# Performance work log

Hardware: AMD Instinct MI355X
Metric: run time of the kernel (lower is better)

## Reference

```python
import jax, jax.numpy as jnp
import numpy as np

B, S, E, H = 8, 1024, 1024, 16
D = E // H  # head_dim = hidden_size // num_heads


def setup_inputs() -> dict:
    key = jax.random.key(0)
    ks = jax.random.split(key, 9)
    s = 0.02
    return {
        "h":  jax.random.normal(ks[0], (B, S, E), jnp.float32),
        # per-head projection weights stacked over heads; torch Linear(E, D) -> stored [E, D] (x @ W)
        "Wq": jax.random.normal(ks[1], (H, E, D), jnp.float32) * s,
        "bq": jax.random.normal(ks[2], (H, D), jnp.float32) * s,
        "Wk": jax.random.normal(ks[3], (H, E, D), jnp.float32) * s,
        "bk": jax.random.normal(ks[4], (H, D), jnp.float32) * s,
        "Wv": jax.random.normal(ks[5], (H, E, D), jnp.float32) * s,  # dead weight: original passes h as value
        "bv": jax.random.normal(ks[6], (H, D), jnp.float32) * s,
        "Wo": jax.random.normal(ks[7], (E, E), jnp.float32) * s,
        "bo": jax.random.normal(ks[8], (E,), jnp.float32) * s,
    }


def reference(h, Wq, bq, Wk, bk, Wv, bv, Wo, bo):
    # Batched over all heads at once instead of the original Python loop.
    q = jnp.einsum('bse,hed->bhsd', h, Wq) + bq[None, :, None, :]   # [B,H,S,D]
    k = jnp.einsum('bse,hed->bhsd', h, Wk) + bk[None, :, None, :]   # [B,H,S,D]
    # v is computed in the original module but NOT used (do_attention gets h as value)
    _v = jnp.einsum('bse,hed->bhsd', h, Wv) + bv[None, :, None, :]
    scale = 1.0 / jnp.sqrt(jnp.asarray(D, h.dtype))
    scores = jnp.einsum('bhsd,bhtd->bhst', q, k) * scale            # [B,H,S,T]
    # original: F.softmax(scores, dim=1) on per-head [B,S,T] -> query axis = axis 2 here
    weights = jax.nn.softmax(scores, axis=2)
    ctx = jnp.einsum('bhst,bte->bhse', weights, h)                  # value = h (embed_dim), per original
    # torch.cat over dim=1 of per-head [B,S,E] outputs -> [B, H*S, E]
    x = ctx.reshape(B, H * S, E)
    return x @ Wo + bo
```

## Files before the change

kernel.cpp:

```cpp
#include <hip/hip_runtime.h>

#define B_ 8
#define S_ 1024
#define E_ 1024
#define H_ 16
#define D_ 64

typedef __attribute__((ext_vector_type(8))) __bf16 bf16x8;
typedef __attribute__((ext_vector_type(4))) float f32x4;
typedef __attribute__((ext_vector_type(4))) unsigned short u16x4;
typedef __attribute__((ext_vector_type(8))) unsigned short u16x8;

static __device__ __forceinline__ unsigned short f2bf_hw(float f) {
  union { __bf16 b; unsigned short u; } v;
  v.b = (__bf16)f;
  return v.u;
}

#if __has_builtin(__builtin_amdgcn_exp2f)
#define EXP2(x) __builtin_amdgcn_exp2f(x)
#else
#define EXP2(x) exp2f(x)
#endif
#define SCALE2 0.18033688f

#define MFMA16(a, b, c) __builtin_amdgcn_mfma_f32_16x16x32_bf16((a), (b), (c), 0, 0, 0)

__global__ void cast_f32_bf16_kernel(const float* __restrict__ src,
                                     unsigned short* __restrict__ dst, int n4) {
  int i = blockIdx.x * 256 + threadIdx.x;
  if (i >= n4) return;
  float4 v = reinterpret_cast<const float4*>(src)[i];
  u16x4 o;
  o[0] = f2bf_hw(v.x); o[1] = f2bf_hw(v.y); o[2] = f2bf_hw(v.z); o[3] = f2bf_hw(v.w);
  reinterpret_cast<u16x4*>(dst)[i] = o;
}

__global__ void transpose_cast_kernel(const float* __restrict__ src,
                                      unsigned short* __restrict__ dst,
                                      int rows, int cols) {
  __shared__ unsigned short tile[64][65];
  const float* s = src + (size_t)blockIdx.z * rows * cols;
  unsigned short* d = dst + (size_t)blockIdx.z * rows * cols;
  int rb = blockIdx.y * 64, cb = blockIdx.x * 64;
#pragma unroll
  for (int k = 0; k < 16; k++) {
    int idx = threadIdx.x + 256 * k;
    int r = idx >> 6, c = idx & 63;
    tile[r][c] = f2bf_hw(s[(size_t)(rb + r) * cols + cb + c]);
  }
  __syncthreads();
#pragma unroll
  for (int k = 0; k < 16; k++) {
    int idx = threadIdx.x + 256 * k;
    int r = idx >> 6, c = idx & 63;
    d[(size_t)(cb + r) * rows + rb + c] = tile[c][r];
  }
}

__launch_bounds__(256)
__global__ void gemm_G_kernel(const unsigned short* __restrict__ hb,
                              const unsigned short* __restrict__ WoT,
                              unsigned short* __restrict__ Gt) {
  int mblk = blockIdx.x, nblk = blockIdx.y, b = blockIdx.z;
  const unsigned short* A = hb + (size_t)b * S_ * E_;
  int tid = threadIdx.x, l = tid & 63, w = tid >> 6;
  int ws = w & 1, wc = w >> 1, lr = l & 15, lg = l >> 4;
  f32x4 acc[4][4] = {};
  int ar[4], bc[4];
#pragma unroll
  for (int i = 0; i < 4; i++) ar[i] = mblk * 128 + ws * 64 + i * 16 + lr;
#pragma unroll
  for (int j = 0; j < 4; j++) bc[j] = nblk * 128 + wc * 64 + j * 16 + lr;
  for (int k0 = 0; k0 < E_; k0 += 32) {
    bf16x8 a[4], bb[4];
#pragma unroll
    for (int i = 0; i < 4; i++)
      a[i] = *reinterpret_cast<const bf16x8*>(A + (size_t)ar[i] * E_ + k0 + lg * 8);
#pragma unroll
    for (int j = 0; j < 4; j++)
      bb[j] = *reinterpret_cast<const bf16x8*>(WoT + (size_t)bc[j] * E_ + k0 + lg * 8);
#pragma unroll
    for (int i = 0; i < 4; i++)
#pragma unroll
      for (int j = 0; j < 4; j++)
        acc[i][j] = MFMA16(a[i], bb[j], acc[i][j]);
  }
#pragma unroll
  for (int i = 0; i < 4; i++) {
    int t0 = mblk * 128 + ws * 64 + i * 16 + lg * 4;
#pragma unroll
    for (int j = 0; j < 4; j++) {
      u16x4 p;
#pragma unroll
      for (int r = 0; r < 4; r++) p[r] = f2bf_hw(acc[i][j][r]);
      int e = bc[j];
      size_t addr = (((size_t)b * 4 + (e >> 8)) * 32 + (t0 >> 5)) * 8192 +
                    (size_t)(e & 255) * 32 + (t0 & 31);
      *reinterpret_cast<u16x4*>(Gt + addr) = p;
    }
  }
}

__launch_bounds__(256)
__global__ void proj_qk_kernel(const unsigned short* __restrict__ hb,
                               const unsigned short* __restrict__ WqT,
                               const unsigned short* __restrict__ WkT,
                               const float* __restrict__ bq,
                               const float* __restrict__ bk,
                               unsigned short* __restrict__ Qb,
                               unsigned short* __restrict__ Kb) {
  int sblk = blockIdx.x, z = blockIdx.y;
  int b = z >> 4, h = z & 15;
  const unsigned short* A = hb + (size_t)b * S_ * E_;
  const unsigned short* Btq = WqT + (size_t)h * D_ * E_;
  const unsigned short* Btk = WkT + (size_t)h * D_ * E_;
  int tid = threadIdx.x, l = tid & 63, w = tid >> 6;
  int ws = w & 1, wc = w >> 1, lr = l & 15, lg = l >> 4;
  f32x4 accq[4][2] = {}, acck[4][2] = {};
  int ar[4], bc[2];
#pragma unroll
  for (int i = 0; i < 4; i++) ar[i] = sblk * 128 + ws * 64 + i * 16 + lr;
#pragma unroll
  for (int j = 0; j < 2; j++) bc[j] = wc * 32 + j * 16 + lr;
  for (int k0 = 0; k0 < E_; k0 += 32) {
    bf16x8 a[4], bbq[2], bbk[2];
#pragma unroll
    for (int i = 0; i < 4; i++)
      a[i] = *reinterpret_cast<const bf16x8*>(A + (size_t)ar[i] * E_ + k0 + lg * 8);
#pragma unroll
    for (int j = 0; j < 2; j++) {
      bbq[j] = *reinterpret_cast<const bf16x8*>(Btq + (size_t)bc[j] * E_ + k0 + lg * 8);
      bbk[j] = *reinterpret_cast<const bf16x8*>(Btk + (size_t)bc[j] * E_ + k0 + lg * 8);
    }
#pragma unroll
    for (int i = 0; i < 4; i++)
#pragma unroll
      for (int j = 0; j < 2; j++) {
        accq[i][j] = MFMA16(a[i], bbq[j], accq[i][j]);
        acck[i][j] = MFMA16(a[i], bbk[j], acck[i][j]);
      }
  }
  unsigned short* oq = Qb + (size_t)z * S_ * D_;
  unsigned short* ok = Kb + (size_t)z * S_ * D_;
#pragma unroll
  for (int j = 0; j < 2; j++) {
    float bvq = bq[h * D_ + bc[j]], bvk = bk[h * D_ + bc[j]];
#pragma unroll
    for (int i = 0; i < 4; i++)
#pragma unroll
      for (int r = 0; r < 4; r++) {
        int s = sblk * 128 + ws * 64 + i * 16 + lg * 4 + r;
        oq[(size_t)s * D_ + bc[j]] = f2bf_hw(accq[i][j][r] + bvq);
        ok[(size_t)s * D_ + bc[j]] = f2bf_hw(acck[i][j][r] + bvk);
      }
  }
}

__launch_bounds__(256)
__global__ void stats_kernel(const unsigned short* __restrict__ Qb,
                             const unsigned short* __restrict__ Kb,
                             float* __restrict__ c) {
  int tblk = blockIdx.x, z = blockIdx.y;
  const unsigned short* Q = Qb + (size_t)z * S_ * D_;
  const unsigned short* K = Kb + (size_t)z * S_ * D_;
  int tid = threadIdx.x, l = tid & 63, w = tid >> 6;
  int lr = l & 15, lg = l >> 4;
  int tb = tblk * 256 + w * 64;
  const float scale = 0.125f;
  bf16x8 kb[4][2];
#pragma unroll
  for (int j = 0; j < 4; j++)
#pragma unroll
    for (int ks = 0; ks < 2; ks++)
      kb[j][ks] = *reinterpret_cast<const bf16x8*>(
          K + (size_t)(tb + j * 16 + lr) * D_ + ks * 32 + lg * 8);
  float m[4], zz[4];
#pragma unroll
  for (int j = 0; j < 4; j++) { m[j] = -1e30f; zz[j] = 0.f; }
  for (int s0 = 0; s0 < S_; s0 += 32) {
    bf16x8 aq[2][2];
#pragma unroll
    for (int sf = 0; sf < 2; sf++)
#pragma unroll
      for (int ks = 0; ks < 2; ks++)
        aq[sf][ks] = *reinterpret_cast<const bf16x8*>(
            Q + (size_t)(s0 + sf * 16 + lr) * D_ + ks * 32 + lg * 8);
    f32x4 acc[2][4] = {};
#pragma unroll
    for (int sf = 0; sf < 2; sf++)
#pragma unroll
      for (int j = 0; j < 4; j++) {
        acc[sf][j] = MFMA16(aq[sf][0], kb[j][0], acc[sf][j]);
        acc[sf][j] = MFMA16(aq[sf][1], kb[j][1], acc[sf][j]);
      }
#pragma unroll
    for (int j = 0; j < 4; j++) {
      float v[8];
#pragma unroll
      for (int sf = 0; sf < 2; sf++)
#pragma unroll
        for (int r = 0; r < 4; r++) v[sf * 4 + r] = acc[sf][j][r] * scale;
      float mx = m[j];
#pragma unroll
      for (int t = 0; t < 8; t++) mx = fmaxf(mx, v[t]);
      float sum = 0.f;
#pragma unroll
      for (int t = 0; t < 8; t++) sum += __expf(v[t] - mx);
      zz[j] = zz[j] * __expf(m[j] - mx) + sum;
      m[j] = mx;
    }
  }
#pragma unroll
  for (int j = 0; j < 4; j++) {
    float mj = m[j], zj = zz[j];
#pragma unroll
    for (int off = 16; off <= 32; off <<= 1) {
      float om = __shfl_xor(mj, off, 64);
      float oz = __shfl_xor(zj, off, 64);
      float mn = fmaxf(mj, om);
      zj = zj * __expf(mj - mn) + oz * __expf(om - mn);
      mj = mn;
    }
    if (l < 16)
      c[(size_t)z * S_ + tb + j * 16 + lr] = (mj + __logf(zj)) * 1.44269504f;
  }
}

__launch_bounds__(256, 3)
__global__ void attn_kernel(const unsigned short* __restrict__ Qb,
                            const unsigned short* __restrict__ Kb,
                            const unsigned short* __restrict__ Gt,
                            const float* __restrict__ cst,
                            const float* __restrict__ bo,
                            float* __restrict__ out) {
  int n = blockIdx.x;
  int b = n & 7, h = (n >> 3) & 15, eblk = (n >> 7) & 3, sblk = n >> 9;
  int z = b * 16 + h;
  __shared__ unsigned short Ks[2][64][72];
  __shared__ unsigned short Ps[2][64][72];
  __shared__ float csm[1024];
  int tid = threadIdx.x, l = tid & 63, w = tid >> 6;
  int lr = l & 15, lg = l >> 4;
  const unsigned short* Q = Qb + (size_t)z * S_ * D_ + (size_t)(sblk * 64) * D_;
  const unsigned short* K = Kb + (size_t)z * S_ * D_;
  const unsigned short* Gb = Gt + (((size_t)b * 4 + eblk) * 32) * 8192;

  bf16x8 q[2];
#pragma unroll
  for (int ks = 0; ks < 2; ks++)
    q[ks] = *reinterpret_cast<const bf16x8*>(
        Q + (size_t)(w * 16 + lr) * D_ + ks * 32 + lg * 8);

  size_t goff[4];
#pragma unroll
  for (int j = 0; j < 4; j++)
    goff[j] = (size_t)(w * 64 + j * 16 + lr) * 32 + lg * 8;

  int krow = tid >> 2, kc16 = (tid & 3) * 16;
  u16x8 kreg0, kreg1;
  bf16x8 v[2][4];

  *reinterpret_cast<f32x4*>(&csm[tid * 4]) =
      *reinterpret_cast<const f32x4*>(cst + (size_t)z * S_ + tid * 4);
  kreg0 = *reinterpret_cast<const u16x8*>(K + (size_t)krow * D_ + kc16);
  kreg1 = *reinterpret_cast<const u16x8*>(K + (size_t)krow * D_ + kc16 + 8);
  *reinterpret_cast<u16x8*>(&Ks[0][krow][kc16]) = kreg0;
  *reinterpret_cast<u16x8*>(&Ks[0][krow][kc16 + 8]) = kreg1;
  kreg0 = *reinterpret_cast<const u16x8*>(K + (size_t)(64 + krow) * D_ + kc16);
  kreg1 = *reinterpret_cast<const u16x8*>(K + (size_t)(64 + krow) * D_ + kc16 + 8);
#pragma unroll
  for (int ks = 0; ks < 2; ks++)
#pragma unroll
    for (int j = 0; j < 4; j++)
      v[ks][j] = *reinterpret_cast<const bf16x8*>(Gb + (size_t)ks * 8192 + goff[j]);
  __syncthreads();

  f32x4 acc[4][4] = {};

#define WINDOW(IT, CUR)                                                           \
  do {                                                                            \
    int t0_ = (IT) * 64;                                                          \
                            \
    *reinterpret_cast<u16x8*>(&Ks[(CUR) ^ 1][krow][kc16]) = kreg0;                \
    *reinterpret_cast<u16x8*>(&Ks[(CUR) ^ 1][krow][kc16 + 8]) = kreg1;            \
    {                                                                             \
      int tk_ = ((IT) + 2) & 15;                                                  \
      kreg0 = *reinterpret_cast<const u16x8*>(                                    \
          K + (size_t)(tk_ * 64 + krow) * D_ + kc16);                             \
      kreg1 = *reinterpret_cast<const u16x8*>(                                    \
          K + (size_t)(tk_ * 64 + krow) * D_ + kc16 + 8);                         \
    }                                                                             \
                                            \
    f32x4 sa_[4];                                                                 \
    _Pragma("unroll") for (int tf = 0; tf < 4; tf++) {                            \
      bf16x8 ka0_ = *reinterpret_cast<const bf16x8*>(                             \
          &Ks[CUR][tf * 16 + lr][lg * 8]);                                        \
      bf16x8 ka1_ = *reinterpret_cast<const bf16x8*>(                             \
          &Ks[CUR][tf * 16 + lr][32 + lg * 8]);                                   \
      f32x4 t_ = {};                                                              \
      t_ = MFMA16(ka0_, q[0], t_);                                                \
      sa_[tf] = MFMA16(ka1_, q[1], t_);                                           \
    }                                                                             \
               \
    if ((IT) > 0) {                                                               \
      __builtin_amdgcn_s_setprio(1);                                              \
      _Pragma("unroll") for (int ks = 0; ks < 2; ks++) {                          \
        bf16x8 ap_[4];                                                            \
        _Pragma("unroll") for (int i = 0; i < 4; i++)                             \
          ap_[i] = *reinterpret_cast<const bf16x8*>(                              \
              &Ps[(CUR) ^ 1][i * 16 + lr][ks * 32 + lg * 8]);                     \
        _Pragma("unroll") for (int i = 0; i < 4; i++)                             \
          _Pragma("unroll") for (int j = 0; j < 4; j++)                           \
            acc[i][j] = MFMA16(ap_[i], v[ks][j], acc[i][j]);                      \
      }                                                                           \
      __builtin_amdgcn_s_setprio(0);                                              \
                                      \
      _Pragma("unroll") for (int ks = 0; ks < 2; ks++)                            \
        _Pragma("unroll") for (int j = 0; j < 4; j++)                             \
          v[ks][j] = *reinterpret_cast<const bf16x8*>(                            \
              Gb + ((size_t)(IT) * 2 + ks) * 8192 + goff[j]);                     \
    }                                                                             \
                                 \
    _Pragma("unroll") for (int tf = 0; tf < 4; tf++) {                            \
      f32x4 cv_ = *reinterpret_cast<const f32x4*>(&csm[t0_ + tf * 16 + lg * 4]);  \
      u16x4 p_;                                                                   \
      _Pragma("unroll") for (int r = 0; r < 4; r++)                               \
        p_[r] = f2bf_hw(EXP2(fmaf(sa_[tf][r], SCALE2, -cv_[r])));                 \
      *reinterpret_cast<u16x4*>(&Ps[CUR][w * 16 + lr][tf * 16 + lg * 4]) = p_;    \
    }                                                                             \
    __syncthreads();                                                              \
  } while (0)

  for (int it2 = 0; it2 < 8; ++it2) {
    WINDOW(it2 * 2, 0);
    WINDOW(it2 * 2 + 1, 1);
  }
#undef WINDOW

  {
#pragma unroll
    for (int ks = 0; ks < 2; ks++) {
      bf16x8 ap_[4];
#pragma unroll
      for (int i = 0; i < 4; i++)
        ap_[i] = *reinterpret_cast<const bf16x8*>(&Ps[1][i * 16 + lr][ks * 32 + lg * 8]);
#pragma unroll
      for (int i = 0; i < 4; i++)
#pragma unroll
        for (int j = 0; j < 4; j++)
          acc[i][j] = MFMA16(ap_[i], v[ks][j], acc[i][j]);
    }
  }

  float bov[4];
#pragma unroll
  for (int j = 0; j < 4; j++) bov[j] = bo[eblk * 256 + w * 64 + j * 16 + lr];
#pragma unroll
  for (int i = 0; i < 4; i++)
#pragma unroll
    for (int j = 0; j < 4; j++)
#pragma unroll
      for (int r = 0; r < 4; r++) {
        int s = sblk * 64 + i * 16 + lg * 4 + r;
        int col = eblk * 256 + w * 64 + j * 16 + lr;
        out[((size_t)b * (H_ * S_) + (size_t)h * S_ + s) * E_ + col] =
            acc[i][j][r] + bov[j];
      }
}

extern "C" void kernel_launch(void* const* d_in, const int* in_sizes, int n_in,
                              void* d_out, int out_size, void* d_ws, size_t ws_size,
                              hipStream_t stream) {
  const float* h  = (const float*)d_in[0];
  const float* Wq = (const float*)d_in[1];
  const float* bq = (const float*)d_in[2];
  const float* Wk = (const float*)d_in[3];
  const float* bk = (const float*)d_in[4];
  const float* Wo = (const float*)d_in[7];
  const float* bo = (const float*)d_in[8];
  float* out = (float*)d_out;

  char* p = (char*)d_ws;
  unsigned short* hb  = (unsigned short*)p; p += (size_t)B_ * S_ * E_ * 2;
  unsigned short* WoT = (unsigned short*)p; p += (size_t)E_ * E_ * 2;
  unsigned short* WqT = (unsigned short*)p; p += (size_t)H_ * D_ * E_ * 2;
  unsigned short* WkT = (unsigned short*)p; p += (size_t)H_ * D_ * E_ * 2;
  unsigned short* Qb  = (unsigned short*)p; p += (size_t)B_ * H_ * S_ * D_ * 2;
  unsigned short* Kb  = (unsigned short*)p; p += (size_t)B_ * H_ * S_ * D_ * 2;
  unsigned short* Gt  = (unsigned short*)p; p += (size_t)B_ * E_ * S_ * 2;
  float*          cst = (float*)p;          p += (size_t)B_ * H_ * S_ * 4;

  int n4 = B_ * S_ * E_ / 4;
  cast_f32_bf16_kernel<<<dim3(n4 / 256), 256, 0, stream>>>(h, hb, n4);
  transpose_cast_kernel<<<dim3(16, 16, 1), 256, 0, stream>>>(Wo, WoT, E_, E_);
  transpose_cast_kernel<<<dim3(1, 16, H_), 256, 0, stream>>>(Wq, WqT, E_, D_);
  transpose_cast_kernel<<<dim3(1, 16, H_), 256, 0, stream>>>(Wk, WkT, E_, D_);
  gemm_G_kernel<<<dim3(8, 8, B_), 256, 0, stream>>>(hb, WoT, Gt);
  proj_qk_kernel<<<dim3(8, B_ * H_), 256, 0, stream>>>(hb, WqT, WkT, bq, bk, Qb, Kb);
  stats_kernel<<<dim3(S_ / 256, B_ * H_), 256, 0, stream>>>(Qb, Kb, cst);
  attn_kernel<<<dim3(8192), 256, 0, stream>>>(Qb, Kb, Gt, cst, bo, out);
}
```

Before: 629.4 us.

## Keep K fragments in registers and swap score-tile ownership across warps

Each warp now loads its own 16-row slice of the K tile straight from global memory into registers and holds all 64 query rows in registers. Before, K was staged through a double-buffered shared-memory tile and each warp held its own query slice. This removes the K shared-memory buffer along with its stores and ds_reads. It also lowers LDS footprint, and the exp/P write is remapped so each warp fills a column band of P. The cost is more Q registers, a global K load issued one tile ahead with less latency slack, and strided P stores that may cause bank conflicts.

```diff
diff --git a/kernel.cpp b/kernel.cpp
--- a/kernel.cpp
+++ b/kernel.cpp
@@ -237,7 +237,6 @@
   int n = blockIdx.x;
   int b = n & 7, h = (n >> 3) & 15, eblk = (n >> 7) & 3, sblk = n >> 9;
   int z = b * 16 + h;
-  __shared__ unsigned short Ks[2][64][72];
   __shared__ unsigned short Ps[2][64][72];
   __shared__ float csm[1024];
   int tid = threadIdx.x, l = tid & 63, w = tid >> 6;
@@ -246,29 +245,29 @@
   const unsigned short* K = Kb + (size_t)z * S_ * D_;
   const unsigned short* Gb = Gt + (((size_t)b * 4 + eblk) * 32) * 8192;
 
-  bf16x8 q[2];
-#pragma unroll
-  for (int ks = 0; ks < 2; ks++)
-    q[ks] = *reinterpret_cast<const bf16x8*>(
-        Q + (size_t)(w * 16 + lr) * D_ + ks * 32 + lg * 8);
-
-  size_t goff[4];
-#pragma unroll
-  for (int j = 0; j < 4; j++)
-    goff[j] = (size_t)(w * 64 + j * 16 + lr) * 32 + lg * 8;
-
-  int krow = tid >> 2, kc16 = (tid & 3) * 16;
-  u16x8 kreg0, kreg1;
-  bf16x8 v[2][4];
-
   *reinterpret_cast<f32x4*>(&csm[tid * 4]) =
       *reinterpret_cast<const f32x4*>(cst + (size_t)z * S_ + tid * 4);
-  kreg0 = *reinterpret_cast<const u16x8*>(K + (size_t)krow * D_ + kc16);
-  kreg1 = *reinterpret_cast<const u16x8*>(K + (size_t)krow * D_ + kc16 + 8);
-  *reinterpret_cast<u16x8*>(&Ks[0][krow][kc16]) = kreg0;
-  *reinterpret_cast<u16x8*>(&Ks[0][krow][kc16 + 8]) = kreg1;
-  kreg0 = *reinterpret_cast<const u16x8*>(K + (size_t)(64 + krow) * D_ + kc16);
-  kreg1 = *reinterpret_cast<const u16x8*>(K + (size_t)(64 + krow) * D_ + kc16 + 8);
+
+  bf16x8 q[4][2];
+#pragma unroll
+  for (int sf = 0; sf < 4; sf++)
+#pragma unroll
+    for (int ks = 0; ks < 2; ks++)
+      q[sf][ks] = *reinterpret_cast<const bf16x8*>(
+          Q + (size_t)(sf * 16 + lr) * D_ + ks * 32 + lg * 8);
+
+  bf16x8 ka[2];
+#pragma unroll
+  for (int ks = 0; ks < 2; ks++)
+    ka[ks] = *reinterpret_cast<const bf16x8*>(
+        K + (size_t)(w * 16 + lr) * D_ + ks * 32 + lg * 8);
+
+  int goff[4];
+#pragma unroll
+  for (int j = 0; j < 4; j++)
+    goff[j] = (w * 64 + j * 16 + lr) * 32 + lg * 8;
+
+  bf16x8 v[2][4];
 #pragma unroll
   for (int ks = 0; ks < 2; ks++)
 #pragma unroll
@@ -281,26 +280,19 @@
 #define WINDOW(IT, CUR)                                                           \
   do {                                                                            \
     int t0_ = (IT) * 64;                                                          \
-                            \
-    *reinterpret_cast<u16x8*>(&Ks[(CUR) ^ 1][krow][kc16]) = kreg0;                \
-    *reinterpret_cast<u16x8*>(&Ks[(CUR) ^ 1][krow][kc16 + 8]) = kreg1;            \
+                        \
+    f32x4 sa_[4];                                                                 \
+    _Pragma("unroll") for (int sf = 0; sf < 4; sf++) {                            \
+      f32x4 t_ = {};                                                              \
+      t_ = MFMA16(ka[0], q[sf][0], t_);                                           \
+      sa_[sf] = MFMA16(ka[1], q[sf][1], t_);                                      \
+    }                                                                             \
+               \
     {                                                                             \
-      int tk_ = ((IT) + 2) & 15;                                                  \
-      kreg0 = *reinterpret_cast<const u16x8*>(                                    \
-          K + (size_t)(tk_ * 64 + krow) * D_ + kc16);                             \
-      kreg1 = *reinterpret_cast<const u16x8*>(                                    \
-          K + (size_t)(tk_ * 64 + krow) * D_ + kc16 + 8);                         \
-    }                                                                             \
-                                            \
-    f32x4 sa_[4];                                                                 \
-    _Pragma("unroll") for (int tf = 0; tf < 4; tf++) {                            \
-      bf16x8 ka0_ = *reinterpret_cast<const bf16x8*>(                             \
-          &Ks[CUR][tf * 16 + lr][lg * 8]);                                        \
-      bf16x8 ka1_ = *reinterpret_cast<const bf16x8*>(                             \
-          &Ks[CUR][tf * 16 + lr][32 + lg * 8]);                                   \
-      f32x4 t_ = {};                                                              \
-      t_ = MFMA16(ka0_, q[0], t_);                                                \
-      sa_[tf] = MFMA16(ka1_, q[1], t_);                                           \
+      int tk_ = ((IT) + 1) & 15;                                                  \
+      _Pragma("unroll") for (int ks = 0; ks < 2; ks++)                            \
+        ka[ks] = *reinterpret_cast<const bf16x8*>(                                \
+            K + (size_t)(tk_ * 64 + w * 16 + lr) * D_ + ks * 32 + lg * 8);        \
     }                                                                             \
                \
     if ((IT) > 0) {                                                               \
@@ -321,13 +313,16 @@
           v[ks][j] = *reinterpret_cast<const bf16x8*>(                            \
               Gb + ((size_t)(IT) * 2 + ks) * 8192 + goff[j]);                     \
     }                                                                             \
-                                 \
-    _Pragma("unroll") for (int tf = 0; tf < 4; tf++) {                            \
-      f32x4 cv_ = *reinterpret_cast<const f32x4*>(&csm[t0_ + tf * 16 + lg * 4]);  \
-      u16x4 p_;                                                                   \
-      _Pragma("unroll") for (int r = 0; r < 4; r++)                               \
-        p_[r] = f2bf_hw(EXP2(fmaf(sa_[tf][r], SCALE2, -cv_[r])));                 \
-      *reinterpret_cast<u16x4*>(&Ps[CUR][w * 16 + lr][tf * 16 + lg * 4]) = p_;    \
+               \
+    {                                                                             \
+      f32x4 cv_ = *reinterpret_cast<const f32x4*>(&csm[t0_ + w * 16 + lg * 4]);   \
+      _Pragma("unroll") for (int sf = 0; sf < 4; sf++) {                          \
+        u16x4 p_;                                                                 \
+        _Pragma("unroll") for (int r = 0; r < 4; r++)                             \
+          p_[r] = f2bf_hw(EXP2(fmaf(sa_[sf][r], SCALE2, -cv_[r])));               \
+        *reinterpret_cast<u16x4*>(                                                \
+            &Ps[CUR][sf * 16 + lr][w * 16 + lg * 4]) = p_;                        \
+      }                                                                           \
     }                                                                             \
     __syncthreads();                                                              \
   } while (0)
```

Result: slower. 1.298 ms (+106.2%).
